# Kernel optimization log

Measured on AMD Instinct MI355X. Metric: run time of the kernel, lower is better.

## Reference

```python
import jax, jax.numpy as jnp
import numpy as np

N, L, H, D, NCLS = 8192, 1024, 512, 256, 2


def setup_inputs() -> dict:
    key = jax.random.key(0)
    ks = jax.random.split(key, 11)
    s = 0.02  # xavier-ish init scale
    return {
        "x": jax.random.normal(ks[0], (N, L), jnp.float32),
        "W_fc": jax.random.normal(ks[1], (L, H), jnp.float32) * s,
        "b_fc": jnp.zeros((H,), jnp.float32),
        "W_a": jax.random.normal(ks[2], (H, D), jnp.float32) * s,
        "b_a": jnp.zeros((D,), jnp.float32),
        "W_b": jax.random.normal(ks[3], (H, D), jnp.float32) * s,
        "b_b": jnp.zeros((D,), jnp.float32),
        "W_c": jax.random.normal(ks[4], (D, 1), jnp.float32) * s,
        "b_c": jnp.zeros((1,), jnp.float32),
        "W_cls": jax.random.normal(ks[5], (H, NCLS), jnp.float32) * s,
        "b_cls": jnp.zeros((NCLS,), jnp.float32),
    }


def reference(x, W_fc, b_fc, W_a, b_a, W_b, b_b, W_c, b_c, W_cls, b_cls):
    n = x.shape[0]
    # fc: Linear + ReLU (dropout p=0, eval)
    h = jax.nn.relu(x @ W_fc + b_fc)                      # [N, 512]
    # gated attention net (Attn_Net_Gated, n_classes=1)
    a = jnp.tanh(h @ W_a + b_a)                           # [N, 256]
    b = jax.nn.sigmoid(h @ W_b + b_b)                     # [N, 256]
    scores = ((a * b) @ W_c + b_c)[:, 0]                  # [N] diagonal scores
    # A_raw: the original's wasteful CxNxN diagonal matrix (C=1)
    idx = jnp.arange(n)
    A_raw = jnp.zeros((1, n, n), x.dtype).at[0, idx, idx].set(scores)
    # bag_forward: softmax over all N*N entries (N^2 - N zeros off-diagonal),
    # then M = (A @ h).sum(dim=1). Closed form, numerically stable:
    m = jnp.maximum(jnp.max(scores), jnp.zeros((), x.dtype))
    e = jnp.exp(scores - m)                               # diag exp terms
    e0 = jnp.exp(-m)                                      # off-diag exp(0 - m)
    Z = jnp.sum(e) + (n * n - n) * e0
    s = e / Z                                             # softmaxed diagonal
    # row_i @ h = s_i*h_i + (1/Z)*sum_{j!=i} h_j ; sum over i:
    M = s @ h + ((n - 1) * e0 / Z) * jnp.sum(h, axis=0)   # [512]
    logits = M @ W_cls + b_cls                            # [2]
    return (logits[None, :], A_raw)
```

## Files before the change

kernel.cpp:

```cpp
#include <hip/hip_runtime.h>
#include <stdint.h>

#define NROWS 8192
#define LDIM  1024
#define HDIM  512

typedef __attribute__((ext_vector_type(8))) short short8;
typedef __attribute__((ext_vector_type(4))) float f32x4;
typedef __attribute__((ext_vector_type(4))) unsigned int u32x4;

typedef __attribute__((address_space(3))) unsigned int lds_uint;
typedef const __attribute__((address_space(1))) unsigned int glob_uint;

#define Z_K1_START 0L
#define ZB_K1      3968
#define Z_G1_START 8126464L
#define ZB_G1      2304
#define Z_G2_START 12845056L
#define ZB_G2      1280
#define Z_RW_START 15466496L
#define ZB_RW      640
#define Z_END      16777215L

__device__ __forceinline__ void llds16(const void* g, void* l) {
  __builtin_amdgcn_global_load_lds((glob_uint*)g, (lds_uint*)l, 16, 0, 0);
}

__device__ __forceinline__ unsigned short f2bf(float f) {
  union { float f; unsigned int u; } c; c.f = f;
  unsigned int u = c.u;
  unsigned int r = (u + 0x7fffu + ((u >> 16) & 1u)) >> 16;
  return (unsigned short)r;
}

__device__ __forceinline__ float bfbits2f(unsigned int hi16) {
  union { unsigned int u; float f; } c; c.u = hi16;
  return c.f;
}

__device__ __forceinline__ void zero_duty(float* __restrict__ out, long zstart, int zblk, int tid) {
  u32x4* out16 = (u32x4*)(out + 4);
  long c0 = zstart + (long)zblk * 2048;
  long c1 = c0 + 2048 < Z_END ? c0 + 2048 : Z_END;
  u32x4 z = {0u, 0u, 0u, 0u};
  for (long i = c0 + tid; i < c1; i += 256) out16[i] = z;
}

__global__ __launch_bounds__(256) void prep_kernel(const float* __restrict__ x,
                                                   const float* __restrict__ Wfc,
                                                   const float* __restrict__ Wa,
                                                   const float* __restrict__ Wb,
                                                   unsigned short* __restrict__ xb,
                                                   unsigned short* __restrict__ WfcT,
                                                   unsigned short* __restrict__ WabT,
                                                   float* __restrict__ out) {
  __shared__ float tile[32][33];
  const int bid = blockIdx.x;
  const int tid = threadIdx.x;
  if (bid < ZB_K1) {
    zero_duty(out, Z_K1_START, bid, tid);
    if (bid == 0 && tid == 0) {
      out[2] = 0.f; out[3] = 0.f;
      out[67108864] = 0.f; out[67108865] = 0.f;
    }
    return;
  }
  if (bid < ZB_K1 + 4096) {
    long i = ((long)(bid - ZB_K1) * 256 + tid) * 8;
    float4 v0 = *(const float4*)(x + i);
    float4 v1 = *(const float4*)(x + i + 4);
    union { unsigned short s[8]; uint4 u; } o;
    o.s[0] = f2bf(v0.x); o.s[1] = f2bf(v0.y); o.s[2] = f2bf(v0.z); o.s[3] = f2bf(v0.w);
    o.s[4] = f2bf(v1.x); o.s[5] = f2bf(v1.y); o.s[6] = f2bf(v1.z); o.s[7] = f2bf(v1.w);
    *(uint4*)(xb + i) = o.u;
    return;
  }
  int tt = bid - (ZB_K1 + 4096);
  const float* src; unsigned short* dst; int srcn, dstk, k0, n0, mode;
  if (tt < 512) {
    src = Wfc; dst = WfcT; srcn = 512; dstk = 1024; mode = 0;
    k0 = (tt >> 4) * 32; n0 = (tt & 15) * 32;
  } else if (tt < 640) {
    int t2 = tt - 512;
    src = Wa; dst = WabT; srcn = 256; dstk = 512; mode = 1;
    k0 = (t2 >> 3) * 32; n0 = (t2 & 7) * 32;
  } else {
    int t2 = tt - 640;
    src = Wb; dst = WabT; srcn = 256; dstk = 512; mode = 2;
    k0 = (t2 >> 3) * 32; n0 = (t2 & 7) * 32;
  }
  int r = tid >> 3, c4 = (tid & 7) * 4;
  float4 v = *(const float4*)(src + (long)(k0 + r) * srcn + n0 + c4);
  tile[r][c4 + 0] = v.x; tile[r][c4 + 1] = v.y; tile[r][c4 + 2] = v.z; tile[r][c4 + 3] = v.w;
  __syncthreads();
  union { unsigned short s[4]; uint2 u; } o;
#pragma unroll
  for (int j = 0; j < 4; ++j) o.s[j] = f2bf(tile[c4 + j][r]);
  int n = n0 + r;
  long crow = (mode == 0) ? (long)n
                          : (long)(((n >> 4) << 5) + (n & 15) + (mode == 2 ? 16 : 0));
  *(uint2*)(dst + crow * dstk + k0 + c4) = o.u;
}

template <int EPI>
__global__ __launch_bounds__(256) void gemm_bt(const unsigned short* __restrict__ A,
                                               const unsigned short* __restrict__ Bt,
                                               const float* __restrict__ q0,
                                               const float* __restrict__ q1,
                                               const float* __restrict__ q2,
                                               void* __restrict__ outp,
                                               int K,
                                               float* __restrict__ zout, long zstart) {
  constexpr int BM = 64, BN = 128, BK = 32;
  __shared__ unsigned short sA[2][BM * BK];
  __shared__ unsigned short sB[2][BN * BK];
  const int tid = threadIdx.x;
  constexpr int nbn = HDIM / BN;
  const int ncomp = (NROWS / BM) * nbn;
  if ((int)blockIdx.x >= ncomp) {
    zero_duty(zout, zstart, (int)blockIdx.x - ncomp, tid);
    return;
  }
  const int lane = tid & 63;
  const int wv = tid >> 6;
  const int wm = wv >> 1;
  const int wn = wv & 1;
  const int bm = blockIdx.x >> 2, bn = blockIdx.x & 3;
  const int row0 = bm * BM, col0 = bn * BN;
  const int nk = K >> 5;
  const int ldsA = (wv * 64) * 8;
  const int arow = tid >> 2, acb = (tid & 3) * 8;

  f32x4 acc[2][4] = {};

  auto stage = [&](int buf, int kt) {
    llds16(A + (long)(row0 + arow) * K + kt * BK + acb, (unsigned short*)&sA[buf][ldsA]);
#pragma unroll
    for (int r = 0; r < 2; ++r) {
      int c = r * 256 + tid;
      llds16(Bt + (long)(col0 + (c >> 2)) * K + kt * BK + (c & 3) * 8,
             (unsigned short*)&sB[buf][(r * 256 + wv * 64) * 8]);
    }
  };

  stage(0, 0);
  __syncthreads();

  for (int kt = 0; kt < nk; ++kt) {
    int cur = kt & 1;
    if (kt + 1 < nk) stage(cur ^ 1, kt + 1);
    const unsigned short* bA = sA[cur];
    const unsigned short* bB = sB[cur];
    short8 af[2], bfr[4];
#pragma unroll
    for (int fm = 0; fm < 2; ++fm)
      af[fm] = *(const short8*)&bA[(wm * 32 + fm * 16 + (lane & 15)) * BK + (lane >> 4) * 8];
#pragma unroll
    for (int fn = 0; fn < 4; ++fn)
      bfr[fn] = *(const short8*)&bB[(wn * 64 + fn * 16 + (lane & 15)) * BK + (lane >> 4) * 8];
#pragma unroll
    for (int fm = 0; fm < 2; ++fm)
#pragma unroll
      for (int fn = 0; fn < 4; ++fn)
        acc[fm][fn] = __builtin_amdgcn_mfma_f32_16x16x32_bf16(af[fm], bfr[fn], acc[fm][fn], 0, 0, 0);
    __syncthreads();
  }

  if (EPI == 0) {
    const float* bias = q0;
    unsigned short* oh = (unsigned short*)outp;
#pragma unroll
    for (int fm = 0; fm < 2; ++fm)
#pragma unroll
      for (int fn = 0; fn < 4; ++fn)
#pragma unroll
        for (int i = 0; i < 4; ++i) {
          int row = row0 + wm * 32 + fm * 16 + (lane >> 4) * 4 + i;
          int col = col0 + wn * 64 + fn * 16 + (lane & 15);
          float v = acc[fm][fn][i] + bias[col];
          v = v > 0.f ? v : 0.f;
          oh[(long)row * HDIM + col] = f2bf(v);
        }
  } else {
    const float* ba_ = q0; const float* bb_ = q1; const float* Wc_ = q2;
#pragma unroll
    for (int g = 0; g < 2; ++g) {
      const int colg = col0 + wn * 64 + g * 32;
      const int d0 = (colg >> 5) * 16 + (lane & 15);
      float wc = Wc_[d0], av = ba_[d0], bv = bb_[d0];
      float* sp = (float*)outp + (long)(colg >> 5) * NROWS;
#pragma unroll
      for (int fm = 0; fm < 2; ++fm)
#pragma unroll
        for (int i = 0; i < 4; ++i) {
          float aa = acc[fm][g * 2 + 0][i] + av;
          float bbv = acc[fm][g * 2 + 1][i] + bv;
          float v = tanhf(aa) * (1.f / (1.f + __expf(-bbv))) * wc;
#pragma unroll
          for (int off = 1; off < 16; off <<= 1) v += __shfl_xor(v, off);
          if ((lane & 15) == 0)
            sp[row0 + wm * 32 + fm * 16 + (lane >> 4) * 4 + i] = v;
        }
    }
  }
}

__global__ __launch_bounds__(256) void redwsum_kernel(const float* __restrict__ spart,
                                                      const float* __restrict__ bc,
                                                      const unsigned short* __restrict__ h,
                                                      float* __restrict__ part,
                                                      float* __restrict__ out) {
  const int b = blockIdx.x;
  const int t = threadIdx.x;
  if (b >= 64) {
    zero_duty(out, Z_RW_START, b - 64, t);
    return;
  }
  __shared__ float sc[NROWS];
  __shared__ float red[256];
  __shared__ float warr[128];
  const float bcv = bc[0];
  float lmax = -1e30f;
  for (int k = t; k < NROWS; k += 256) {
    float s = bcv;
#pragma unroll
    for (int q = 0; q < 16; ++q) s += spart[q * NROWS + k];
    sc[k] = s;
    lmax = fmaxf(lmax, s);
  }
  red[t] = lmax; __syncthreads();
  for (int s = 128; s; s >>= 1) { if (t < s) red[t] = fmaxf(red[t], red[t + s]); __syncthreads(); }
  float m = fmaxf(red[0], 0.f);
  __syncthreads();
  float lsum = 0.f;
  for (int k = t; k < NROWS; k += 256) lsum += __expf(sc[k] - m);
  red[t] = lsum; __syncthreads();
  for (int s = 128; s; s >>= 1) { if (t < s) red[t] += red[t + s]; __syncthreads(); }
  float e0 = __expf(-m);
  float Z = red[0] + 67100672.0f * e0;
  float c0w = 8191.0f * e0 / Z;
  if (t < 128) warr[t] = __expf(sc[b * 128 + t] - m) / Z + c0w;
  __syncthreads();
  float a0 = 0.f, a1 = 0.f;
  for (int i = 0; i < 128; ++i) {
    float wi = warr[i];
    unsigned int hv = *(const unsigned int*)&h[(long)(b * 128 + i) * 512 + t * 2];
    a0 += wi * bfbits2f(hv << 16);
    a1 += wi * bfbits2f(hv & 0xffff0000u);
  }
  part[b * 512 + t * 2] = a0;
  part[b * 512 + t * 2 + 1] = a1;
}

__global__ __launch_bounds__(512) void final_kernel(const float* __restrict__ part,
                                                    const float* __restrict__ spart,
                                                    const float* __restrict__ bc,
                                                    const float* __restrict__ Wcls,
                                                    const float* __restrict__ bcls,
                                                    float* __restrict__ out) {
  const int t = threadIdx.x;
  if (blockIdx.x > 0) {
    if (t < 256) {
      int row = (blockIdx.x - 1) * 256 + t;
      float s = bc[0];
#pragma unroll
      for (int q = 0; q < 16; ++q) s += spart[q * NROWS + row];
      out[2 + 8193L * row] = s;
    }
    return;
  }
  __shared__ float Msh[512];
  float s = 0.f;
  for (int b = 0; b < 64; ++b) s += part[b * 512 + t];
  Msh[t] = s;
  __syncthreads();
  if (t < 64) {
    float p0 = 0.f, p1 = 0.f;
    for (int j = t; j < 512; j += 64) { p0 += Msh[j] * Wcls[j * 2]; p1 += Msh[j] * Wcls[j * 2 + 1]; }
#pragma unroll
    for (int off = 32; off; off >>= 1) { p0 += __shfl_down(p0, off); p1 += __shfl_down(p1, off); }
    if (t == 0) { out[0] = p0 + bcls[0]; out[1] = p1 + bcls[1]; }
  }
}

extern "C" void kernel_launch(void* const* d_in, const int* in_sizes, int n_in,
                              void* d_out, int out_size, void* d_ws, size_t ws_size,
                              hipStream_t stream) {
  const float* x    = (const float*)d_in[0];
  const float* Wfc  = (const float*)d_in[1];
  const float* bfc  = (const float*)d_in[2];
  const float* Wa   = (const float*)d_in[3];
  const float* ba   = (const float*)d_in[4];
  const float* Wb   = (const float*)d_in[5];
  const float* bb   = (const float*)d_in[6];
  const float* Wc   = (const float*)d_in[7];
  const float* bc   = (const float*)d_in[8];
  const float* Wcls = (const float*)d_in[9];
  const float* bcls = (const float*)d_in[10];
  float* out = (float*)d_out;
  char* ws = (char*)d_ws;

  unsigned short* xb    = (unsigned short*)(ws + 0);
  unsigned short* WfcT  = (unsigned short*)(ws + 16777216);
  unsigned short* WabT  = (unsigned short*)(ws + 17825792);
  unsigned short* hbuf  = (unsigned short*)(ws + 18350080);
  float*          spart = (float*)(ws + 26738688);
  float*          part  = (float*)(ws + 27262976);

  prep_kernel<<<ZB_K1 + 4096 + 768, 256, 0, stream>>>(x, Wfc, Wa, Wb, xb, WfcT, WabT, out);
  gemm_bt<0><<<512 + ZB_G1, 256, 0, stream>>>(xb, WfcT, bfc, nullptr, nullptr, hbuf, LDIM, out, Z_G1_START);
  gemm_bt<1><<<512 + ZB_G2, 256, 0, stream>>>(hbuf, WabT, ba, bb, Wc, spart, HDIM, out, Z_G2_START);
  redwsum_kernel<<<64 + ZB_RW, 256, 0, stream>>>(spart, bc, hbuf, part, out);
  final_kernel<<<33, 512, 0, stream>>>(part, spart, bc, Wcls, bcls, out);
}
```

Measured before the change: 115.3 us.

## Fuse x fp32-to-bf16 conversion into first GEMM and swizzle LDS tiles

Removes the separate pass that converted x to bf16 in the prep kernel. The first GEMM now loads fp32 x tiles straight into LDS and packs them to bf16 when building fragments, which saves a full write and re-read of the 16 MB converted buffer. Both GEMMs gain XOR-swizzled LDS layouts to cut bank conflicts, and the zero-fill work for the large output is rebalanced across kernels. The cost is twice the LDS traffic for the A operand, extra conversion ALU inside the GEMM main loop, and a cheaper round-to-nearest that does not break ties to even.

Result: slower. 123.8 us (+7.4%).

```diff
diff --git a/kernel.cpp b/kernel.cpp
--- a/kernel.cpp
+++ b/kernel.cpp
@@ -15,11 +15,11 @@
 #define Z_K1_START 0L
 #define ZB_K1      3968
 #define Z_G1_START 8126464L
-#define ZB_G1      2304
-#define Z_G2_START 12845056L
-#define ZB_G2      1280
-#define Z_RW_START 15466496L
-#define ZB_RW      640
+#define ZB_G1      2560
+#define Z_G2_START 13369344L
+#define ZB_G2      1408
+#define Z_RW_START 16252928L
+#define ZB_RW      256
 #define Z_END      16777215L
 
 __device__ __forceinline__ void llds16(const void* g, void* l) {
@@ -31,6 +31,11 @@
   unsigned int u = c.u;
   unsigned int r = (u + 0x7fffu + ((u >> 16) & 1u)) >> 16;
   return (unsigned short)r;
+}
+
+__device__ __forceinline__ unsigned int pkbf(float a, float b) {
+  union { float f; unsigned int u; } ca, cb; ca.f = a; cb.f = b;
+  return ((ca.u + 0x8000u) >> 16) | ((cb.u + 0x8000u) & 0xffff0000u);
 }
 
 __device__ __forceinline__ float bfbits2f(unsigned int hi16) {
@@ -46,11 +51,9 @@
   for (long i = c0 + tid; i < c1; i += 256) out16[i] = z;
 }
 
-__global__ __launch_bounds__(256) void prep_kernel(const float* __restrict__ x,
-                                                   const float* __restrict__ Wfc,
+__global__ __launch_bounds__(256) void prep_kernel(const float* __restrict__ Wfc,
                                                    const float* __restrict__ Wa,
                                                    const float* __restrict__ Wb,
-                                                   unsigned short* __restrict__ xb,
                                                    unsigned short* __restrict__ WfcT,
                                                    unsigned short* __restrict__ WabT,
                                                    float* __restrict__ out) {
@@ -65,17 +68,7 @@
     }
     return;
   }
-  if (bid < ZB_K1 + 4096) {
-    long i = ((long)(bid - ZB_K1) * 256 + tid) * 8;
-    float4 v0 = *(const float4*)(x + i);
-    float4 v1 = *(const float4*)(x + i + 4);
-    union { unsigned short s[8]; uint4 u; } o;
-    o.s[0] = f2bf(v0.x); o.s[1] = f2bf(v0.y); o.s[2] = f2bf(v0.z); o.s[3] = f2bf(v0.w);
-    o.s[4] = f2bf(v1.x); o.s[5] = f2bf(v1.y); o.s[6] = f2bf(v1.z); o.s[7] = f2bf(v1.w);
-    *(uint4*)(xb + i) = o.u;
-    return;
-  }
-  int tt = bid - (ZB_K1 + 4096);
+  int tt = bid - ZB_K1;
   const float* src; unsigned short* dst; int srcn, dstk, k0, n0, mode;
   if (tt < 512) {
     src = Wfc; dst = WfcT; srcn = 512; dstk = 1024; mode = 0;
@@ -102,43 +95,124 @@
   *(uint2*)(dst + crow * dstk + k0 + c4) = o.u;
 }
 
-template <int EPI>
-__global__ __launch_bounds__(256) void gemm_bt(const unsigned short* __restrict__ A,
-                                               const unsigned short* __restrict__ Bt,
-                                               const float* __restrict__ q0,
-                                               const float* __restrict__ q1,
-                                               const float* __restrict__ q2,
-                                               void* __restrict__ outp,
-                                               int K,
-                                               float* __restrict__ zout, long zstart) {
-  constexpr int BM = 64, BN = 128, BK = 32;
-  __shared__ unsigned short sA[2][BM * BK];
-  __shared__ unsigned short sB[2][BN * BK];
+__global__ __launch_bounds__(256) void gemm1_kernel(const float* __restrict__ X,
+                                                    const unsigned short* __restrict__ Bt,
+                                                    const float* __restrict__ bias,
+                                                    unsigned short* __restrict__ out,
+                                                    float* __restrict__ zout) {
+  constexpr int K = LDIM, nk = K / 32;
+  __shared__ float sA[2][64 * 32];
+  __shared__ unsigned short sB[2][128 * 32];
   const int tid = threadIdx.x;
-  constexpr int nbn = HDIM / BN;
-  const int ncomp = (NROWS / BM) * nbn;
-  if ((int)blockIdx.x >= ncomp) {
-    zero_duty(zout, zstart, (int)blockIdx.x - ncomp, tid);
+  if ((int)blockIdx.x >= 512) {
+    zero_duty(zout, Z_G1_START, (int)blockIdx.x - 512, tid);
     return;
   }
   const int lane = tid & 63;
   const int wv = tid >> 6;
-  const int wm = wv >> 1;
-  const int wn = wv & 1;
+  const int wm = wv >> 1, wn = wv & 1;
   const int bm = blockIdx.x >> 2, bn = blockIdx.x & 3;
-  const int row0 = bm * BM, col0 = bn * BN;
-  const int nk = K >> 5;
-  const int ldsA = (wv * 64) * 8;
-  const int arow = tid >> 2, acb = (tid & 3) * 8;
+  const int row0 = bm * 64, col0 = bn * 128;
 
   f32x4 acc[2][4] = {};
 
   auto stage = [&](int buf, int kt) {
-    llds16(A + (long)(row0 + arow) * K + kt * BK + acb, (unsigned short*)&sA[buf][ldsA]);
 #pragma unroll
     for (int r = 0; r < 2; ++r) {
       int c = r * 256 + tid;
-      llds16(Bt + (long)(col0 + (c >> 2)) * K + kt * BK + (c & 3) * 8,
+      int ar = c >> 3, as = (c & 7) ^ (ar & 7);
+      llds16(X + (long)(row0 + ar) * K + kt * 32 + as * 4,
+             (float*)&sA[buf][(r * 256 + wv * 64) * 4]);
+      int br = c >> 2, bs = (c & 3) ^ ((br >> 1) & 3);
+      llds16(Bt + (long)(col0 + br) * K + kt * 32 + bs * 8,
+             (unsigned short*)&sB[buf][(r * 256 + wv * 64) * 8]);
+    }
+  };
+
+  stage(0, 0);
+  __syncthreads();
+
+  for (int kt = 0; kt < nk; ++kt) {
+    int cur = kt & 1;
+    if (kt + 1 < nk) stage(cur ^ 1, kt + 1);
+    const float* bA = sA[cur];
+    const unsigned short* bB = sB[cur];
+    short8 af[2], bfr[4];
+#pragma unroll
+    for (int fm = 0; fm < 2; ++fm) {
+      int r = wm * 32 + fm * 16 + (lane & 15);
+      int g = r & 7;
+      int s0 = (lane >> 4) * 2;
+      float4 f0 = *(const float4*)&bA[r * 32 + ((s0)     ^ g) * 4];
+      float4 f1 = *(const float4*)&bA[r * 32 + ((s0 + 1) ^ g) * 4];
+      union { unsigned int u[4]; short8 s8; } o;
+      o.u[0] = pkbf(f0.x, f0.y); o.u[1] = pkbf(f0.z, f0.w);
+      o.u[2] = pkbf(f1.x, f1.y); o.u[3] = pkbf(f1.z, f1.w);
+      af[fm] = o.s8;
+    }
+#pragma unroll
+    for (int fn = 0; fn < 4; ++fn) {
+      int rb = wn * 64 + fn * 16 + (lane & 15);
+      int sb = (lane >> 4) ^ ((rb >> 1) & 3);
+      bfr[fn] = *(const short8*)&bB[rb * 32 + sb * 8];
+    }
+#pragma unroll
+    for (int fm = 0; fm < 2; ++fm)
+#pragma unroll
+      for (int fn = 0; fn < 4; ++fn)
+        acc[fm][fn] = __builtin_amdgcn_mfma_f32_16x16x32_bf16(af[fm], bfr[fn], acc[fm][fn], 0, 0, 0);
+    __syncthreads();
+  }
+
+  const float* bias_ = bias;
+#pragma unroll
+  for (int fm = 0; fm < 2; ++fm)
+#pragma unroll
+    for (int fn = 0; fn < 4; ++fn)
+#pragma unroll
+      for (int i = 0; i < 4; ++i) {
+        int row = row0 + wm * 32 + fm * 16 + (lane >> 4) * 4 + i;
+        int col = col0 + wn * 64 + fn * 16 + (lane & 15);
+        float v = acc[fm][fn][i] + bias_[col];
+        v = v > 0.f ? v : 0.f;
+        out[(long)row * HDIM + col] = f2bf(v);
+      }
+}
+
+__global__ __launch_bounds__(256) void gemm2_kernel(const unsigned short* __restrict__ A,
+                                                    const unsigned short* __restrict__ Bt,
+                                                    const float* __restrict__ ba_,
+                                                    const float* __restrict__ bb_,
+                                                    const float* __restrict__ Wc_,
+                                                    float* __restrict__ spart,
+                                                    float* __restrict__ zout) {
+  constexpr int K = HDIM, nk = K / 32;
+  __shared__ unsigned short sA[2][64 * 32];
+  __shared__ unsigned short sB[2][128 * 32];
+  const int tid = threadIdx.x;
+  if ((int)blockIdx.x >= 512) {
+    zero_duty(zout, Z_G2_START, (int)blockIdx.x - 512, tid);
+    return;
+  }
+  const int lane = tid & 63;
+  const int wv = tid >> 6;
+  const int wm = wv >> 1, wn = wv & 1;
+  const int bm = blockIdx.x >> 2, bn = blockIdx.x & 3;
+  const int row0 = bm * 64, col0 = bn * 128;
+
+  f32x4 acc[2][4] = {};
+
+  auto stage = [&](int buf, int kt) {
+    {
+      int ar = tid >> 2, as = (tid & 3) ^ ((ar >> 1) & 3);
+      llds16(A + (long)(row0 + ar) * K + kt * 32 + as * 8,
+             (unsigned short*)&sA[buf][(wv * 64) * 8]);
+    }
+#pragma unroll
+    for (int r = 0; r < 2; ++r) {
+      int c = r * 256 + tid;
+      int br = c >> 2, bs = (c & 3) ^ ((br >> 1) & 3);
+      llds16(Bt + (long)(col0 + br) * K + kt * 32 + bs * 8,
              (unsigned short*)&sB[buf][(r * 256 + wv * 64) * 8]);
     }
   };
@@ -153,11 +227,17 @@
     const unsigned short* bB = sB[cur];
     short8 af[2], bfr[4];
 #pragma unroll
-    for (int fm = 0; fm < 2; ++fm)
-      af[fm] = *(const short8*)&bA[(wm * 32 + fm * 16 + (lane & 15)) * BK + (lane >> 4) * 8];
-#pragma unroll
-    for (int fn = 0; fn < 4; ++fn)
-      bfr[fn] = *(const short8*)&bB[(wn * 64 + fn * 16 + (lane & 15)) * BK + (lane >> 4) * 8];
+    for (int fm = 0; fm < 2; ++fm) {
+      int r = wm * 32 + fm * 16 + (lane & 15);
+      int s = (lane >> 4) ^ ((r >> 1) & 3);
+      af[fm] = *(const short8*)&bA[r * 32 + s * 8];
+    }
+#pragma unroll
+    for (int fn = 0; fn < 4; ++fn) {
+      int rb = wn * 64 + fn * 16 + (lane & 15);
+      int sb = (lane >> 4) ^ ((rb >> 1) & 3);
+      bfr[fn] = *(const short8*)&bB[rb * 32 + sb * 8];
+    }
 #pragma unroll
     for (int fm = 0; fm < 2; ++fm)
 #pragma unroll
@@ -166,42 +246,24 @@
     __syncthreads();
   }
 
-  if (EPI == 0) {
-    const float* bias = q0;
-    unsigned short* oh = (unsigned short*)outp;
+#pragma unroll
+  for (int g = 0; g < 2; ++g) {
+    const int colg = col0 + wn * 64 + g * 32;
+    const int d0 = (colg >> 5) * 16 + (lane & 15);
+    float wc = Wc_[d0], av = ba_[d0], bv = bb_[d0];
+    float* sp = spart + (long)(colg >> 5) * NROWS;
 #pragma unroll
     for (int fm = 0; fm < 2; ++fm)
 #pragma unroll
-      for (int fn = 0; fn < 4; ++fn)
-#pragma unroll
-        for (int i = 0; i < 4; ++i) {
-          int row = row0 + wm * 32 + fm * 16 + (lane >> 4) * 4 + i;
-          int col = col0 + wn * 64 + fn * 16 + (lane & 15);
-          float v = acc[fm][fn][i] + bias[col];
-          v = v > 0.f ? v : 0.f;
-          oh[(long)row * HDIM + col] = f2bf(v);
-        }
-  } else {
-    const float* ba_ = q0; const float* bb_ = q1; const float* Wc_ = q2;
-#pragma unroll
-    for (int g = 0; g < 2; ++g) {
-      const int colg = col0 + wn * 64 + g * 32;
-      const int d0 = (colg >> 5) * 16 + (lane & 15);
-      float wc = Wc_[d0], av = ba_[d0], bv = bb_[d0];
-      float* sp = (float*)outp + (long)(colg >> 5) * NROWS;
-#pragma unroll
-      for (int fm = 0; fm < 2; ++fm)
-#pragma unroll
-        for (int i = 0; i < 4; ++i) {
-          float aa = acc[fm][g * 2 + 0][i] + av;
-          float bbv = acc[fm][g * 2 + 1][i] + bv;
-          float v = tanhf(aa) * (1.f / (1.f + __expf(-bbv))) * wc;
-#pragma unroll
-          for (int off = 1; off < 16; off <<= 1) v += __shfl_xor(v, off);
-          if ((lane & 15) == 0)
-            sp[row0 + wm * 32 + fm * 16 + (lane >> 4) * 4 + i] = v;
-        }
-    }
+      for (int i = 0; i < 4; ++i) {
+        float aa = acc[fm][g * 2 + 0][i] + av;
+        float bbv = acc[fm][g * 2 + 1][i] + bv;
+        float v = tanhf(aa) * (1.f / (1.f + __expf(-bbv))) * wc;
+#pragma unroll
+        for (int off = 1; off < 16; off <<= 1) v += __shfl_xor(v, off);
+        if ((lane & 15) == 0)
+          sp[row0 + wm * 32 + fm * 16 + (lane >> 4) * 4 + i] = v;
+      }
   }
 }
 
@@ -300,16 +362,15 @@
   float* out = (float*)d_out;
   char* ws = (char*)d_ws;
 
-  unsigned short* xb    = (unsigned short*)(ws + 0);
-  unsigned short* WfcT  = (unsigned short*)(ws + 16777216);
-  unsigned short* WabT  = (unsigned short*)(ws + 17825792);
-  unsigned short* hbuf  = (unsigned short*)(ws + 18350080);
-  float*          spart = (float*)(ws + 26738688);
-  float*          part  = (float*)(ws + 27262976);
-
-  prep_kernel<<<ZB_K1 + 4096 + 768, 256, 0, stream>>>(x, Wfc, Wa, Wb, xb, WfcT, WabT, out);
-  gemm_bt<0><<<512 + ZB_G1, 256, 0, stream>>>(xb, WfcT, bfc, nullptr, nullptr, hbuf, LDIM, out, Z_G1_START);
-  gemm_bt<1><<<512 + ZB_G2, 256, 0, stream>>>(hbuf, WabT, ba, bb, Wc, spart, HDIM, out, Z_G2_START);
+  unsigned short* WfcT  = (unsigned short*)(ws + 0);
+  unsigned short* WabT  = (unsigned short*)(ws + 1048576);
+  unsigned short* hbuf  = (unsigned short*)(ws + 1572864);
+  float*          spart = (float*)(ws + 9961472);
+  float*          part  = (float*)(ws + 10485760);
+
+  prep_kernel<<<ZB_K1 + 768, 256, 0, stream>>>(Wfc, Wa, Wb, WfcT, WabT, out);
+  gemm1_kernel<<<512 + ZB_G1, 256, 0, stream>>>(x, WfcT, bfc, hbuf, out);
+  gemm2_kernel<<<512 + ZB_G2, 256, 0, stream>>>(hbuf, WabT, ba, bb, Wc, spart, out);
   redwsum_kernel<<<64 + ZB_RW, 256, 0, stream>>>(spart, bc, hbuf, part, out);
   final_kernel<<<33, 512, 0, stream>>>(part, spart, bc, Wcls, bcls, out);
 }
```
